# Kernel optimization log

Measured on AMD Instinct MI355X. Metric: run time of the kernel, lower is better.

Reference implementation:

```python
import jax, jax.numpy as jnp
import numpy as np

LN_EPS = 1e-5  # torch.nn.LayerNorm default


def setup_inputs() -> dict:
    key = jax.random.key(0)
    ks = jax.random.split(key, 6)
    b, e, c, h, w, m = 4, 16, 256, 32, 64, 1024
    return {
        "x": jax.random.normal(ks[0], (b, e, c, h, w), dtype=jnp.float32),
        "ln_w": jnp.ones((c, h, w), dtype=jnp.float32),
        "ln_b": jnp.zeros((c, h, w), dtype=jnp.float32),
        "w_in": jax.random.normal(ks[1], (c, m), dtype=jnp.float32) * (1.0 / np.sqrt(c)),
        "b_in": jax.random.normal(ks[2], (m,), dtype=jnp.float32) * 0.01,
        "w_out": jax.random.normal(ks[3], (m, c), dtype=jnp.float32) * (1.0 / np.sqrt(m)),
        "b_out": jax.random.normal(ks[4], (c,), dtype=jnp.float32) * 0.01,
        "gamma": jnp.full((c,), 1e-6, dtype=jnp.float32),
    }


def reference(x, ln_w, ln_b, w_in, b_in, w_out, b_out, gamma):
    # LayerNorm over the last 3 dims (c, h, w) with affine params of shape (c, h, w)
    mu = jnp.mean(x, axis=(-3, -2, -1), keepdims=True)
    var = jnp.var(x, axis=(-3, -2, -1), keepdims=True)  # biased, matches torch
    y = (x - mu) * jax.lax.rsqrt(var + LN_EPS)
    y = y * ln_w + ln_b  # broadcast (c,h,w) over (b,e,...)

    # b e c h w -> b e h w c
    y = jnp.moveaxis(y, 2, -1)
    t = jax.nn.gelu(y @ w_in + b_in, approximate=False)  # torch GELU is exact erf
    t = (t @ w_out + b_out) * gamma  # layer scale on channel dim

    # b e h w c -> b e c h w, residual add
    return x + jnp.moveaxis(t, -1, 2)
```

## Files before the change

kernel.cpp:

```cpp
#include <hip/hip_runtime.h>
#include <math.h>

#define NS 64
#define CD 256
#define HW 2048
#define MD 1024
#define SAMPLE (CD * HW)
#define LN_EPS 1e-5f

#define PB 64
#define MC 32
#define NCH (MD / MC)

typedef float f32x4 __attribute__((ext_vector_type(4)));
typedef long i64;

__device__ __forceinline__ int swz(int p) {
  int k = (p ^ (p >> 2)) & 15;
  return ((k & 7) << 4) | (k & 8);
}

__device__ __forceinline__ void gl_lds16(const unsigned char* g, unsigned char* l) {
  __builtin_amdgcn_global_load_lds(
      (const __attribute__((address_space(1))) unsigned char*)g,
      (__attribute__((address_space(3))) unsigned char*)l, 16, 0, 0);
}

__global__ __launch_bounds__(256) void k_prep(const float* __restrict__ w_in,
                                              const float* __restrict__ w_out,
                                              unsigned char* __restrict__ w_in8p,
                                              unsigned char* __restrict__ w_out8p) {
  int id = blockIdx.x * 256 + threadIdx.x;
  if (id < 65536) {
    int i = id;
    int f = i >> 7, l = (i >> 1) & 63, j0 = (i & 1) * 4;
    int m = (f >> 3) * 16 + (l & 15);
    int c0 = (f & 7) * 32 + (l >> 4) * 8 + j0;
    float a = w_in[(size_t)(c0 + 0) * MD + m];
    float b = w_in[(size_t)(c0 + 1) * MD + m];
    float c = w_in[(size_t)(c0 + 2) * MD + m];
    float d = w_in[(size_t)(c0 + 3) * MD + m];
    int r = __builtin_amdgcn_cvt_pk_fp8_f32(a, b, 0, false);
    r = __builtin_amdgcn_cvt_pk_fp8_f32(c, d, r, true);
    ((int*)w_in8p)[i] = r;
  } else {
    int i = id - 65536;
    int g = i >> 7, l = (i >> 1) & 63, j0 = (i & 1) * 4;
    int c = (g & 15) * 16 + (l & 15);
    int m0 = (g >> 4) * 32 + (l >> 4) * 8 + j0;
    float a = w_out[(size_t)(m0 + 0) * CD + c];
    float b = w_out[(size_t)(m0 + 1) * CD + c];
    float cc = w_out[(size_t)(m0 + 2) * CD + c];
    float d = w_out[(size_t)(m0 + 3) * CD + c];
    int r = __builtin_amdgcn_cvt_pk_fp8_f32(a, b, 0, false);
    r = __builtin_amdgcn_cvt_pk_fp8_f32(cc, d, r, true);
    ((int*)w_out8p)[i] = r;
  }
}

__global__ __launch_bounds__(256) void k_stats1(const float* __restrict__ x,
                                                double* __restrict__ partial) {
  int s = blockIdx.x >> 3, sl = blockIdx.x & 7;
  const float4* p = (const float4*)(x + (size_t)s * SAMPLE + (size_t)sl * 65536);
  double sum = 0.0, ssq = 0.0;
  for (int i = 0; i < 64; ++i) {
    float4 v = p[i * 256 + threadIdx.x];
    sum += (double)v.x + (double)v.y + (double)v.z + (double)v.w;
    ssq += (double)v.x * v.x + (double)v.y * v.y + (double)v.z * v.z + (double)v.w * v.w;
  }
  for (int off = 32; off; off >>= 1) {
    sum += __shfl_down(sum, off);
    ssq += __shfl_down(ssq, off);
  }
  __shared__ double red[4][2];
  int wv = threadIdx.x >> 6, ln = threadIdx.x & 63;
  if (ln == 0) { red[wv][0] = sum; red[wv][1] = ssq; }
  __syncthreads();
  if (threadIdx.x == 0) {
    for (int i = 1; i < 4; ++i) { sum += red[i][0]; ssq += red[i][1]; }
    partial[blockIdx.x * 2] = sum;
    partial[blockIdx.x * 2 + 1] = ssq;
  }
}

__global__ void k_stats2(const double* __restrict__ partial, float* __restrict__ stats) {
  int s = threadIdx.x;
  double sum = 0.0, ssq = 0.0;
  for (int i = 0; i < 8; ++i) {
    sum += partial[(s * 8 + i) * 2];
    ssq += partial[(s * 8 + i) * 2 + 1];
  }
  double mean = sum / (double)SAMPLE;
  double var = ssq / (double)SAMPLE - mean * mean;
  stats[s * 2] = (float)mean;
  stats[s * 2 + 1] = (float)(1.0 / sqrt(var + (double)LN_EPS));
}

__global__ __launch_bounds__(512, 6) void k_fused(
    const float* __restrict__ x, const float* __restrict__ ln_w, const float* __restrict__ ln_b,
    const float* __restrict__ b_in, const float* __restrict__ b_out, const float* __restrict__ gamma,
    const unsigned char* __restrict__ w_in8p, const unsigned char* __restrict__ w_out8p,
    const float* __restrict__ stats, float* __restrict__ out) {
  __shared__ unsigned char smem[45056];
  unsigned char* Ysh = smem + 8192;

  const int tid = threadIdx.x;
  const int lane = tid & 63, l15 = lane & 15, l4 = lane >> 4;
  const int wv = tid >> 6;
  const int q = wv >> 1, h = wv & 1;
  const int s = blockIdx.x >> 5;
  const int p0 = (blockIdx.x & 31) * PB;
  const float mu = stats[s * 2], rstd = stats[s * 2 + 1];
  const float a_ln = rstd, c_ln = -mu * rstd;
  const size_t xbase = (size_t)s * SAMPLE;

  gl_lds16(w_in8p + wv * 1024 + lane * 16, smem + 24576 + wv * 1024);
  gl_lds16(w_out8p + wv * 1024 + lane * 16, smem + wv * 1024);

  #pragma unroll
  for (int it = 0; it < 2; ++it) {
    int bid = it * 512 + tid;
    int c0 = (bid >> 4) * 4, pp = (bid & 15) * 4;
    float yv[4][4];
    #pragma unroll
    for (int i = 0; i < 4; ++i) {
      size_t off = (size_t)(c0 + i) * HW + p0 + pp;
      float4 xv = *(const float4*)(x + xbase + off);
      float4 lw = *(const float4*)(ln_w + off);
      float4 lb = *(const float4*)(ln_b + off);
      yv[i][0] = fmaf(fmaf(xv.x, a_ln, c_ln), lw.x, lb.x);
      yv[i][1] = fmaf(fmaf(xv.y, a_ln, c_ln), lw.y, lb.y);
      yv[i][2] = fmaf(fmaf(xv.z, a_ln, c_ln), lw.z, lb.z);
      yv[i][3] = fmaf(fmaf(xv.w, a_ln, c_ln), lw.w, lb.w);
    }
    #pragma unroll
    for (int j = 0; j < 4; ++j) {
      int p = pp + j;
      int r = __builtin_amdgcn_cvt_pk_fp8_f32(yv[0][j], yv[1][j], 0, false);
      r = __builtin_amdgcn_cvt_pk_fp8_f32(yv[2][j], yv[3][j], r, true);
      *(int*)&Ysh[p * 256 + (c0 ^ swz(p))] = r;
    }
  }

  const int strip = q * 16;
  const int pY = strip + l15;
  const int sY = swz(pY);
  f32x4 acc2[8] = {};

  __syncthreads();

  i64 breg[8];
  #pragma unroll
  for (int kk = 0; kk < 8; ++kk)
    breg[kk] = *(const i64*)&Ysh[pY * 256 + ((kk * 32 + l4 * 8) ^ sY)];

  __syncthreads();

  for (int ch = 0; ch < NCH; ++ch) {
    if (ch) __syncthreads();

    if (ch + 1 < NCH) {
      const size_t co = (size_t)(ch + 1) * 8192;
      gl_lds16(w_in8p + co + wv * 1024 + lane * 16,
               smem + 24576 + ((ch + 1) & 1) * 8192 + wv * 1024);
      gl_lds16(w_out8p + co + wv * 1024 + lane * 16,
               smem + ((ch + 1) % 3) * 8192 + wv * 1024);
    }

    __builtin_amdgcn_s_setprio(1);
    if (ch) {
      const i64 a2 = *(const i64*)(smem + 40960 + ((ch - 1) & 1) * 2048 +
                                   q * 512 + l15 * 32 + l4 * 8);
      const unsigned char* W2 = smem + ((ch - 1) % 3) * 8192;
      #pragma unroll
      for (int cti = 0; cti < 8; ++cti) {
        i64 b2 = *(const i64*)&W2[(h * 8 + cti) * 512 + lane * 8];
        acc2[cti] = __builtin_amdgcn_mfma_f32_16x16x32_fp8_fp8(a2, b2, acc2[cti], 0, 0, 0);
      }
    }

    const unsigned char* W1 = smem + 24576 + (ch & 1) * 8192;
    f32x4 acc1 = {};
    #pragma unroll
    for (int kk = 0; kk < 8; ++kk) {
      i64 a = *(const i64*)&W1[(h * 8 + kk) * 512 + lane * 8];
      acc1 = __builtin_amdgcn_mfma_f32_16x16x32_fp8_fp8(a, breg[kk], acc1, 0, 0, 0);
    }
    __builtin_amdgcn_s_setprio(0);

    {
      const float4 bi = *(const float4*)&b_in[ch * 32 + h * 16 + l4 * 4];
      float g[4];
      #pragma unroll
      for (int r = 0; r < 4; ++r) {
        float t = acc1[r] + ((const float*)&bi)[r];
        g[r] = t * __builtin_amdgcn_rcpf(1.0f + __expf(-1.702f * t));
      }
      int pk = __builtin_amdgcn_cvt_pk_fp8_f32(g[0], g[1], 0, false);
      pk = __builtin_amdgcn_cvt_pk_fp8_f32(g[2], g[3], pk, true);
      *(int*)(smem + 40960 + (ch & 1) * 2048 + q * 512 + l15 * 32 + h * 16 + l4 * 4) = pk;
    }
  }

  __syncthreads();
  {
    const i64 a2 = *(const i64*)(smem + 40960 + ((NCH - 1) & 1) * 2048 +
                                 q * 512 + l15 * 32 + l4 * 8);
    const unsigned char* W2 = smem + ((NCH - 1) % 3) * 8192;
    #pragma unroll
    for (int cti = 0; cti < 8; ++cti) {
      i64 b2 = *(const i64*)&W2[(h * 8 + cti) * 512 + lane * 8];
      acc2[cti] = __builtin_amdgcn_mfma_f32_16x16x32_fp8_fp8(a2, b2, acc2[cti], 0, 0, 0);
    }
  }

  #pragma unroll
  for (int cti = 0; cti < 8; ++cti) {
    int cc = h * 128 + cti * 16 + l15;
    float gm = gamma[cc], bo = b_out[cc];
    int p = p0 + strip + l4 * 4;
    size_t off = xbase + (size_t)cc * HW + p;
    float4 xv = *(const float4*)(x + off);
    float4 o;
    #pragma unroll
    for (int r = 0; r < 4; ++r)
      ((float*)&o)[r] = ((const float*)&xv)[r] + gm * (acc2[cti][r] + bo);
    *(float4*)(out + off) = o;
  }
}

extern "C" void kernel_launch(void* const* d_in, const int* in_sizes, int n_in,
                              void* d_out, int out_size, void* d_ws, size_t ws_size,
                              hipStream_t stream) {
  const float* x = (const float*)d_in[0];
  const float* ln_w = (const float*)d_in[1];
  const float* ln_b = (const float*)d_in[2];
  const float* w_in = (const float*)d_in[3];
  const float* b_in = (const float*)d_in[4];
  const float* w_out = (const float*)d_in[5];
  const float* b_out = (const float*)d_in[6];
  const float* gamma = (const float*)d_in[7];
  float* out = (float*)d_out;

  char* ws = (char*)d_ws;
  unsigned char* w_in8p = (unsigned char*)ws;
  unsigned char* w_out8p = (unsigned char*)(ws + 262144);
  double* partial = (double*)(ws + 524288);
  float* stats = (float*)(ws + 524288 + 8192);

  k_prep<<<512, 256, 0, stream>>>(w_in, w_out, w_in8p, w_out8p);
  k_stats1<<<512, 256, 0, stream>>>(x, partial);
  k_stats2<<<1, 64, 0, stream>>>(partial, stats);

  k_fused<<<2048, 512, 0, stream>>>(x, ln_w, ln_b, b_in, b_out, gamma,
                                    w_in8p, w_out8p, stats, out);
}
```

Before: 176.7 us.

## Merge prep and stats kernels, split MFMA chains, swizzle GELU exchange buffer

Merges the weight-conversion kernel and the partial-statistics kernel into one launch, so one kernel launch and one serialization point go away. In the fused kernel, the first GEMM's eight dependent MFMAs become two independent accumulator chains. The GELU result is now written before the second GEMM's MFMAs are issued, with the read of the previous chunk hoisted ahead. The hidden-activation exchange buffer gets an XOR swizzle on writes and reads to cut LDS bank conflicts. Splitting the chain adds a little register pressure and an extra add per element.

```diff
diff --git a/kernel.cpp b/kernel.cpp
--- a/kernel.cpp
+++ b/kernel.cpp
@@ -26,60 +26,59 @@
       (__attribute__((address_space(3))) unsigned char*)l, 16, 0, 0);
 }
 
-__global__ __launch_bounds__(256) void k_prep(const float* __restrict__ w_in,
-                                              const float* __restrict__ w_out,
-                                              unsigned char* __restrict__ w_in8p,
-                                              unsigned char* __restrict__ w_out8p) {
-  int id = blockIdx.x * 256 + threadIdx.x;
-  if (id < 65536) {
-    int i = id;
-    int f = i >> 7, l = (i >> 1) & 63, j0 = (i & 1) * 4;
-    int m = (f >> 3) * 16 + (l & 15);
-    int c0 = (f & 7) * 32 + (l >> 4) * 8 + j0;
-    float a = w_in[(size_t)(c0 + 0) * MD + m];
-    float b = w_in[(size_t)(c0 + 1) * MD + m];
-    float c = w_in[(size_t)(c0 + 2) * MD + m];
-    float d = w_in[(size_t)(c0 + 3) * MD + m];
-    int r = __builtin_amdgcn_cvt_pk_fp8_f32(a, b, 0, false);
-    r = __builtin_amdgcn_cvt_pk_fp8_f32(c, d, r, true);
-    ((int*)w_in8p)[i] = r;
+__global__ __launch_bounds__(256) void k_prep_stats(
+    const float* __restrict__ x, const float* __restrict__ w_in,
+    const float* __restrict__ w_out, unsigned char* __restrict__ w_in8p,
+    unsigned char* __restrict__ w_out8p, double* __restrict__ partial) {
+  if (blockIdx.x < 512) {
+    int s = blockIdx.x >> 3, sl = blockIdx.x & 7;
+    const float4* p = (const float4*)(x + (size_t)s * SAMPLE + (size_t)sl * 65536);
+    double sum = 0.0, ssq = 0.0;
+    for (int i = 0; i < 64; ++i) {
+      float4 v = p[i * 256 + threadIdx.x];
+      sum += (double)v.x + (double)v.y + (double)v.z + (double)v.w;
+      ssq += (double)v.x * v.x + (double)v.y * v.y + (double)v.z * v.z + (double)v.w * v.w;
+    }
+    for (int off = 32; off; off >>= 1) {
+      sum += __shfl_down(sum, off);
+      ssq += __shfl_down(ssq, off);
+    }
+    __shared__ double red[4][2];
+    int wv = threadIdx.x >> 6, ln = threadIdx.x & 63;
+    if (ln == 0) { red[wv][0] = sum; red[wv][1] = ssq; }
+    __syncthreads();
+    if (threadIdx.x == 0) {
+      for (int i = 1; i < 4; ++i) { sum += red[i][0]; ssq += red[i][1]; }
+      partial[blockIdx.x * 2] = sum;
+      partial[blockIdx.x * 2 + 1] = ssq;
+    }
   } else {
-    int i = id - 65536;
-    int g = i >> 7, l = (i >> 1) & 63, j0 = (i & 1) * 4;
-    int c = (g & 15) * 16 + (l & 15);
-    int m0 = (g >> 4) * 32 + (l >> 4) * 8 + j0;
-    float a = w_out[(size_t)(m0 + 0) * CD + c];
-    float b = w_out[(size_t)(m0 + 1) * CD + c];
-    float cc = w_out[(size_t)(m0 + 2) * CD + c];
-    float d = w_out[(size_t)(m0 + 3) * CD + c];
-    int r = __builtin_amdgcn_cvt_pk_fp8_f32(a, b, 0, false);
-    r = __builtin_amdgcn_cvt_pk_fp8_f32(cc, d, r, true);
-    ((int*)w_out8p)[i] = r;
-  }
-}
-
-__global__ __launch_bounds__(256) void k_stats1(const float* __restrict__ x,
-                                                double* __restrict__ partial) {
-  int s = blockIdx.x >> 3, sl = blockIdx.x & 7;
-  const float4* p = (const float4*)(x + (size_t)s * SAMPLE + (size_t)sl * 65536);
-  double sum = 0.0, ssq = 0.0;
-  for (int i = 0; i < 64; ++i) {
-    float4 v = p[i * 256 + threadIdx.x];
-    sum += (double)v.x + (double)v.y + (double)v.z + (double)v.w;
-    ssq += (double)v.x * v.x + (double)v.y * v.y + (double)v.z * v.z + (double)v.w * v.w;
-  }
-  for (int off = 32; off; off >>= 1) {
-    sum += __shfl_down(sum, off);
-    ssq += __shfl_down(ssq, off);
-  }
-  __shared__ double red[4][2];
-  int wv = threadIdx.x >> 6, ln = threadIdx.x & 63;
-  if (ln == 0) { red[wv][0] = sum; red[wv][1] = ssq; }
-  __syncthreads();
-  if (threadIdx.x == 0) {
-    for (int i = 1; i < 4; ++i) { sum += red[i][0]; ssq += red[i][1]; }
-    partial[blockIdx.x * 2] = sum;
-    partial[blockIdx.x * 2 + 1] = ssq;
+    int id = (blockIdx.x - 512) * 256 + threadIdx.x;
+    if (id < 65536) {
+      int i = id;
+      int f = i >> 7, l = (i >> 1) & 63, j0 = (i & 1) * 4;
+      int m = (f >> 3) * 16 + (l & 15);
+      int c0 = (f & 7) * 32 + (l >> 4) * 8 + j0;
+      float a = w_in[(size_t)(c0 + 0) * MD + m];
+      float b = w_in[(size_t)(c0 + 1) * MD + m];
+      float c = w_in[(size_t)(c0 + 2) * MD + m];
+      float d = w_in[(size_t)(c0 + 3) * MD + m];
+      int r = __builtin_amdgcn_cvt_pk_fp8_f32(a, b, 0, false);
+      r = __builtin_amdgcn_cvt_pk_fp8_f32(c, d, r, true);
+      ((int*)w_in8p)[i] = r;
+    } else {
+      int i = id - 65536;
+      int g = i >> 7, l = (i >> 1) & 63, j0 = (i & 1) * 4;
+      int c = (g & 15) * 16 + (l & 15);
+      int m0 = (g >> 4) * 32 + (l >> 4) * 8 + j0;
+      float a = w_out[(size_t)(m0 + 0) * CD + c];
+      float b = w_out[(size_t)(m0 + 1) * CD + c];
+      float cc = w_out[(size_t)(m0 + 2) * CD + c];
+      float d = w_out[(size_t)(m0 + 3) * CD + c];
+      int r = __builtin_amdgcn_cvt_pk_fp8_f32(a, b, 0, false);
+      r = __builtin_amdgcn_cvt_pk_fp8_f32(cc, d, r, true);
+      ((int*)w_out8p)[i] = r;
+    }
   }
 }
 
@@ -156,6 +155,10 @@
 
   __syncthreads();
 
+  const int exw = ((((h * 16 + l4 * 4) >> 3) ^ (l15 >> 2)) << 3) + ((l4 & 1) * 4);
+  const int exw_off = 40960 + q * 512 + l15 * 32 + exw;
+  const int exr_off = 40960 + q * 512 + l15 * 32 + ((l4 ^ (l15 >> 2)) << 3);
+
   for (int ch = 0; ch < NCH; ++ch) {
     if (ch) __syncthreads();
 
@@ -167,45 +170,49 @@
                smem + ((ch + 1) % 3) * 8192 + wv * 1024);
     }
 
+    i64 a2 = 0;
+    if (ch) a2 = *(const i64*)(smem + ((ch - 1) & 1) * 2048 + exr_off);
+
+    const unsigned char* W1 = smem + 24576 + (ch & 1) * 8192;
+    f32x4 acc1a = {}, acc1b = {};
     __builtin_amdgcn_s_setprio(1);
+    #pragma unroll
+    for (int kk = 0; kk < 4; ++kk) {
+      i64 a = *(const i64*)&W1[(h * 8 + kk) * 512 + lane * 8];
+      i64 b = *(const i64*)&W1[(h * 8 + 4 + kk) * 512 + lane * 8];
+      acc1a = __builtin_amdgcn_mfma_f32_16x16x32_fp8_fp8(a, breg[kk], acc1a, 0, 0, 0);
+      acc1b = __builtin_amdgcn_mfma_f32_16x16x32_fp8_fp8(b, breg[4 + kk], acc1b, 0, 0, 0);
+    }
+    __builtin_amdgcn_s_setprio(0);
+
+    {
+      const float4 bi = *(const float4*)&b_in[ch * 32 + h * 16 + l4 * 4];
+      float g[4];
+      #pragma unroll
+      for (int r = 0; r < 4; ++r) {
+        float t = acc1a[r] + acc1b[r] + ((const float*)&bi)[r];
+        g[r] = t * __builtin_amdgcn_rcpf(1.0f + __expf(-1.702f * t));
+      }
+      int pk = __builtin_amdgcn_cvt_pk_fp8_f32(g[0], g[1], 0, false);
+      pk = __builtin_amdgcn_cvt_pk_fp8_f32(g[2], g[3], pk, true);
+      *(int*)(smem + (ch & 1) * 2048 + exw_off) = pk;
+    }
+
     if (ch) {
-      const i64 a2 = *(const i64*)(smem + 40960 + ((ch - 1) & 1) * 2048 +
-                                   q * 512 + l15 * 32 + l4 * 8);
       const unsigned char* W2 = smem + ((ch - 1) % 3) * 8192;
+      __builtin_amdgcn_s_setprio(1);
       #pragma unroll
       for (int cti = 0; cti < 8; ++cti) {
         i64 b2 = *(const i64*)&W2[(h * 8 + cti) * 512 + lane * 8];
         acc2[cti] = __builtin_amdgcn_mfma_f32_16x16x32_fp8_fp8(a2, b2, acc2[cti], 0, 0, 0);
       }
-    }
-
-    const unsigned char* W1 = smem + 24576 + (ch & 1) * 8192;
-    f32x4 acc1 = {};
-    #pragma unroll
-    for (int kk = 0; kk < 8; ++kk) {
-      i64 a = *(const i64*)&W1[(h * 8 + kk) * 512 + lane * 8];
-      acc1 = __builtin_amdgcn_mfma_f32_16x16x32_fp8_fp8(a, breg[kk], acc1, 0, 0, 0);
-    }
-    __builtin_amdgcn_s_setprio(0);
-
-    {
-      const float4 bi = *(const float4*)&b_in[ch * 32 + h * 16 + l4 * 4];
-      float g[4];
-      #pragma unroll
-      for (int r = 0; r < 4; ++r) {
-        float t = acc1[r] + ((const float*)&bi)[r];
-        g[r] = t * __builtin_amdgcn_rcpf(1.0f + __expf(-1.702f * t));
-      }
-      int pk = __builtin_amdgcn_cvt_pk_fp8_f32(g[0], g[1], 0, false);
-      pk = __builtin_amdgcn_cvt_pk_fp8_f32(g[2], g[3], pk, true);
-      *(int*)(smem + 40960 + (ch & 1) * 2048 + q * 512 + l15 * 32 + h * 16 + l4 * 4) = pk;
+      __builtin_amdgcn_s_setprio(0);
     }
   }
 
   __syncthreads();
   {
-    const i64 a2 = *(const i64*)(smem + 40960 + ((NCH - 1) & 1) * 2048 +
-                                 q * 512 + l15 * 32 + l4 * 8);
+    const i64 a2 = *(const i64*)(smem + ((NCH - 1) & 1) * 2048 + exr_off);
     const unsigned char* W2 = smem + ((NCH - 1) % 3) * 8192;
     #pragma unroll
     for (int cti = 0; cti < 8; ++cti) {
@@ -248,8 +255,7 @@
   double* partial = (double*)(ws + 524288);
   float* stats = (float*)(ws + 524288 + 8192);
 
-  k_prep<<<512, 256, 0, stream>>>(w_in, w_out, w_in8p, w_out8p);
-  k_stats1<<<512, 256, 0, stream>>>(x, partial);
+  k_prep_stats<<<1024, 256, 0, stream>>>(x, w_in, w_out, w_in8p, w_out8p, partial);
   k_stats2<<<1, 64, 0, stream>>>(partial, stats);
 
   k_fused<<<2048, 512, 0, stream>>>(x, ln_w, ln_b, b_in, b_out, gamma,
```

Measured after the change: 173.8 us. No clear change (-1.7%).
